# Optimization experiments

Hardware: AMD Instinct MI355X
Metric: run time of the kernel (lower is better)

## Reference

```python
import jax, jax.numpy as jnp
import numpy as np

R = 16       # voxel resolution
CH = 64      # channels
NSAMPLE = 16
PROJ = 3


def _bn(x, p, eps):
    # p: [4, C] rows = (gamma, beta, running_mean, running_var); eval-mode BN
    g, b, m, v = p
    sh = [1] * x.ndim
    sh[1] = -1
    return (x - m.reshape(sh)) * (g.reshape(sh) * jax.lax.rsqrt(v.reshape(sh) + eps)) + b.reshape(sh)


def _gather_ch(x, flat_idx):
    # x: [B, C, M], flat_idx: [B, L] -> [B, C, L]
    B, C, _ = x.shape
    idx = jnp.broadcast_to(flat_idx[:, None, :], (B, C, flat_idx.shape[1]))
    return jnp.take_along_axis(x, idx, axis=2)


def _pvb_forward(x, xyz, idx, w3d1, b3d1, bn3d1, w3d2, b3d2, bn3d2, proj_w1, proj_bn, proj_w2, pt_bn):
    B, C, N = x.shape
    r = R
    # ---------- voxelization (coords detached, normalize=False) ----------
    nc = xyz - xyz.mean(axis=2, keepdims=True)
    nc = jnp.clip((nc + 1.0) * 0.5 * r, 0.0, r - 1.0)
    nc = jax.lax.stop_gradient(nc)                        # [B,3,N] float in [0, r-1]
    vi = jnp.round(nc).astype(jnp.int32)
    flat = (vi[:, 0] * r + vi[:, 1]) * r + vi[:, 2]       # [B,N]
    seg = (flat + jnp.arange(B, dtype=jnp.int32)[:, None] * (r ** 3)).reshape(-1)
    feats = x.transpose(0, 2, 1).reshape(B * N, C)
    sums = jax.ops.segment_sum(feats, seg, num_segments=B * r ** 3)
    cnts = jax.ops.segment_sum(jnp.ones((B * N,), x.dtype), seg, num_segments=B * r ** 3)
    v = (sums / jnp.maximum(cnts, 1.0)[:, None]).reshape(B, r, r, r, C).transpose(0, 4, 1, 2, 3)
    # ---------- depthwise Conv3d -> BN3d -> LeakyReLU (x2) ----------
    dn = ('NCDHW', 'OIDHW', 'NCDHW')
    v = jax.lax.conv_general_dilated(v, w3d1, (1, 1, 1), 'SAME', dimension_numbers=dn,
                                     feature_group_count=C) + b3d1.reshape(1, C, 1, 1, 1)
    v = jax.nn.leaky_relu(_bn(v, bn3d1, 1e-4), 0.1)
    v = jax.lax.conv_general_dilated(v, w3d2, (1, 1, 1), 'SAME', dimension_numbers=dn,
                                     feature_group_count=C) + b3d2.reshape(1, C, 1, 1, 1)
    v = jax.nn.leaky_relu(_bn(v, bn3d2, 1e-4), 0.1)
    # ---------- trilinear devoxelize ----------
    vf = v.reshape(B, C, r ** 3)
    lo = jnp.floor(nc).astype(jnp.int32)
    fr = nc - lo
    hi = jnp.minimum(lo + 1, r - 1)
    p_v_x = jnp.zeros((B, C, N), x.dtype)
    for dx in (0, 1):
        for dy in (0, 1):
            for dz in (0, 1):
                xi = hi[:, 0] if dx else lo[:, 0]
                yi = hi[:, 1] if dy else lo[:, 1]
                zi = hi[:, 2] if dz else lo[:, 2]
                w = ((fr[:, 0] if dx else 1.0 - fr[:, 0]) *
                     (fr[:, 1] if dy else 1.0 - fr[:, 1]) *
                     (fr[:, 2] if dz else 1.0 - fr[:, 2]))
                p_v_x = p_v_x + w[:, None, :] * _gather_ch(vf, (xi * r + yi) * r + zi)
    # ---------- neighbor gather (precomputed ball-query idx) ----------
    K = idx.shape[-1]
    flat_nb = idx.reshape(B, N * K)
    x_j = _gather_ch(x, flat_nb).reshape(B, C, N, K)
    xyz_j = _gather_ch(xyz, flat_nb).reshape(B, 3, N, K)
    dp1 = xyz_j - xyz[:, :, :, None]                      # [B,3,N,K]
    df = x_j - x[:, :, :, None]                           # [B,C,N,K]
    # proj_conv: 1x1 conv -> BN2d -> ReLU -> 1x1 conv
    h = jnp.einsum('oc,bcnk->bonk', proj_w1, df)
    h = jax.nn.relu(_bn(h, proj_bn, 1e-5))
    dp2 = jnp.einsum('oc,bcnk->bonk', proj_w2, h)         # [B,3,N,K]
    dp = jnp.concatenate([dp1, dp2], axis=1)              # [B,6,N,K]
    # repeat_interleave of the 6 channels up to C (last gets remainder)
    part = 6
    rep = C // part
    repeats = np.array([rep] * (part - 1) + [C - rep * (part - 1)])
    w = jnp.repeat(dp, repeats, axis=1, total_repeat_length=C)
    x_j = x_j * w
    x_j = jax.nn.relu(_bn(x_j, pt_bn, 1e-5))              # proj_transform
    p_p_x = x_j.max(axis=-1)                              # max-pool over neighbors
    return p_v_x + p_p_x                                  # agg_way == 'add'


def setup_inputs() -> dict:
    key = jax.random.key(0)
    ks = jax.random.split(key, 16)
    B, C, N, K = 4, CH, 16384, NSAMPLE

    def bn_params(k, c):
        k1, k2, k3, k4 = jax.random.split(k, 4)
        return jnp.stack([1.0 + 0.1 * jax.random.normal(k1, (c,), jnp.float32),
                          0.1 * jax.random.normal(k2, (c,), jnp.float32),
                          0.1 * jax.random.normal(k3, (c,), jnp.float32),
                          jax.random.uniform(k4, (c,), jnp.float32, 0.5, 1.5)])

    return dict(
        x=jax.random.normal(ks[0], (B, C, N), jnp.float32),
        xyz=jax.random.uniform(ks[1], (B, 3, N), jnp.float32, -1.0, 1.0),
        idx=jax.random.randint(ks[2], (B, N, K), 0, N, jnp.int32),
        w3d1=0.1 * jax.random.normal(ks[3], (C, 1, 3, 3, 3), jnp.float32),
        b3d1=0.01 * jax.random.normal(ks[4], (C,), jnp.float32),
        bn3d1=bn_params(ks[5], C),
        w3d2=0.1 * jax.random.normal(ks[6], (C, 1, 3, 3, 3), jnp.float32),
        b3d2=0.01 * jax.random.normal(ks[7], (C,), jnp.float32),
        bn3d2=bn_params(ks[8], C),
        proj_w1=0.1 * jax.random.normal(ks[9], (PROJ, C), jnp.float32),
        proj_bn=bn_params(ks[10], PROJ),
        proj_w2=0.3 * jax.random.normal(ks[11], (PROJ, PROJ), jnp.float32),
        pt_bn=bn_params(ks[12], C),
    )


def reference(x, xyz, idx, w3d1, b3d1, bn3d1, w3d2, b3d2, bn3d2, proj_w1, proj_bn, proj_w2, pt_bn):
    return _pvb_forward(x, xyz, idx, w3d1, b3d1, bn3d1, w3d2, b3d2, bn3d2, proj_w1, proj_bn, proj_w2, pt_bn)
```

## Files before the change

### kernel.cpp

```cpp
#include <hip/hip_runtime.h>

namespace {
constexpr int B_  = 4;
constexpr int C_  = 64;
constexpr int N_  = 16384;
constexpr int K_  = 16;
constexpr int R3_ = 4096;

constexpr int OFF_MEANS = 0;
constexpr int OFF_XT    = 16;
constexpr int OFF_PTS   = OFF_XT  + B_*N_*C_/2;
constexpr int OFF_SUMS  = OFF_PTS + B_*N_*8;
constexpr int OFF_CNTS  = OFF_SUMS + B_*R3_*C_;
constexpr int OFF_VOX2  = OFF_CNTS + B_*R3_;
constexpr int FILL_FLOATS = B_*R3_*C_ + B_*R3_;
constexpr int FILL_BLOCKS = FILL_FLOATS / (256 * 4);
}

__device__ __forceinline__ unsigned short f2bf(float f) {
  unsigned u = __float_as_uint(f);
  return (unsigned short)((u + 0x7FFFu + ((u >> 16) & 1u)) >> 16);
}
__device__ __forceinline__ float bf2f(unsigned short h) {
  return __uint_as_float(((unsigned)h) << 16);
}
__device__ __forceinline__ unsigned cvtpk_bf16(float lo, float hi) {
  unsigned r;
  asm("v_cvt_pk_bf16_f32 %0, %1, %2" : "=v"(r) : "v"(lo), "v"(hi));
  return r;
}

__global__ __launch_bounds__(256) void k_init(
    const float* __restrict__ xyz, float* __restrict__ means,
    float* __restrict__ fill) {
  const int blk = blockIdx.x;
  if (blk >= 12) {
    const int base = (blk - 12) * (256 * 4) + threadIdx.x * 4;
    *(float4*)(fill + base) = make_float4(0.f, 0.f, 0.f, 0.f);
    return;
  }
  __shared__ double red[256];
  const float* p = xyz + blk * N_;
  double s = 0.0;
  for (int i = threadIdx.x; i < N_; i += 256) s += (double)p[i];
  red[threadIdx.x] = s;
  __syncthreads();
  for (int st = 128; st; st >>= 1) {
    if (threadIdx.x < st) red[threadIdx.x] += red[threadIdx.x + st];
    __syncthreads();
  }
  if (threadIdx.x == 0) means[blk] = (float)(red[0] * (1.0 / (double)N_));
}

__global__ __launch_bounds__(256) void k_prep(
    const float* __restrict__ x, const float* __restrict__ xyz,
    const float* __restrict__ pw1, const float* __restrict__ means,
    unsigned short* __restrict__ xT, float* __restrict__ pts,
    float* __restrict__ sums, float* __restrict__ cnts) {
  __shared__ float tile[64 * 65];
  __shared__ float ncs[3][64];
  __shared__ int   flats[64];

  const int t   = threadIdx.x;
  const int blk = blockIdx.x;
  const int b   = blk >> 8;
  const int n0  = (blk & 255) << 6;

#pragma unroll
  for (int i = 0; i < 16; ++i) {
    int c = i * 4 + (t >> 6);
    int j = t & 63;
    tile[c * 65 + j] = x[((size_t)(b * C_ + c)) * N_ + n0 + j];
  }
  __syncthreads();

#pragma unroll
  for (int i = 0; i < 16; ++i) {
    int p = i * 4 + (t >> 6);
    int c = t & 63;
    xT[((size_t)(b * N_ + n0 + p)) * C_ + c] = f2bf(tile[c * 65 + p]);
  }

  if (t < 192) {
    int p = t & 63, q = t >> 6;
    float s = 0.f;
#pragma unroll
    for (int c = 0; c < 64; ++c) s = fmaf(pw1[q * 64 + c], tile[c * 65 + p], s);
    size_t pb = ((size_t)(b * N_ + n0 + p)) * 8;
    pts[pb + 3 + q] = s;
    float v = xyz[((size_t)(b * 3 + q)) * N_ + n0 + p];
    pts[pb + q] = v;
    float nc = fminf(fmaxf((v - means[b * 3 + q] + 1.0f) * 8.0f, 0.0f), 15.0f);
    ncs[q][p] = nc;
  } else {
    int p = t & 63;
    size_t pb = ((size_t)(b * N_ + n0 + p)) * 8;
    pts[pb + 6] = 0.f;
    pts[pb + 7] = 0.f;
  }
  __syncthreads();

  if (t < 64) {
    int vx = (int)rintf(ncs[0][t]);
    int vy = (int)rintf(ncs[1][t]);
    int vz = (int)rintf(ncs[2][t]);
    int f = (vx * 16 + vy) * 16 + vz;
    flats[t] = f;
    atomicAdd(&cnts[b * R3_ + f], 1.0f);
  }
  __syncthreads();

  const int w = t >> 6, lane = t & 63;
#pragma unroll
  for (int i = 0; i < 16; ++i) {
    int p = w * 16 + i;
    int f = flats[p];
    atomicAdd(&sums[((size_t)(b * R3_ + f)) * C_ + lane], tile[lane * 65 + p]);
  }
}

__global__ __launch_bounds__(256) void k_conv(
    const float* __restrict__ sums, const float* __restrict__ cnts,
    const float* __restrict__ w3d1, const float* __restrict__ b3d1,
    const float* __restrict__ bn1, const float* __restrict__ w3d2,
    const float* __restrict__ b3d2, const float* __restrict__ bn2,
    unsigned short* __restrict__ vox2) {
  __shared__ float va[18 * 18 * 18];
  __shared__ float vb[18 * 18 * 18];
  const int t = threadIdx.x;
  const int b = blockIdx.x >> 6;
  const int c = blockIdx.x & 63;

  float W1[27], W2[27];
#pragma unroll
  for (int i = 0; i < 27; ++i) { W1[i] = w3d1[c * 27 + i]; W2[i] = w3d2[c * 27 + i]; }
  float s1 = bn1[c] / sqrtf(bn1[192 + c] + 1e-4f);
  float d1 = (b3d1[c] - bn1[128 + c]) * s1 + bn1[64 + c];
  float s2 = bn2[c] / sqrtf(bn2[192 + c] + 1e-4f);
  float d2 = (b3d2[c] - bn2[128 + c]) * s2 + bn2[64 + c];

  for (int i = t; i < 18 * 18 * 18; i += 256) { va[i] = 0.f; vb[i] = 0.f; }
  __syncthreads();

#pragma unroll
  for (int i = 0; i < 16; ++i) {
    int vox = t + i * 256;
    int z = vox & 15, y = (vox >> 4) & 15, xx = vox >> 8;
    float cnt = cnts[b * R3_ + vox];
    float v = sums[((size_t)(b * R3_ + vox)) * C_ + c] / fmaxf(cnt, 1.0f);
    va[((xx + 1) * 18 + (y + 1)) * 18 + (z + 1)] = v;
  }
  __syncthreads();

#pragma unroll
  for (int i = 0; i < 16; ++i) {
    int vox = t + i * 256;
    int z = vox & 15, y = (vox >> 4) & 15, xx = vox >> 8;
    int base = ((xx + 1) * 18 + (y + 1)) * 18 + (z + 1);
    float acc = 0.f;
#pragma unroll
    for (int dx = -1; dx <= 1; ++dx)
#pragma unroll
      for (int dy = -1; dy <= 1; ++dy)
#pragma unroll
        for (int dz = -1; dz <= 1; ++dz)
          acc = fmaf(W1[((dx + 1) * 3 + (dy + 1)) * 3 + (dz + 1)],
                     va[base + dx * 324 + dy * 18 + dz], acc);
    float tt = acc * s1 + d1;
    vb[base] = tt > 0.f ? tt : 0.1f * tt;
  }
  __syncthreads();

#pragma unroll
  for (int i = 0; i < 16; ++i) {
    int vox = t + i * 256;
    int z = vox & 15, y = (vox >> 4) & 15, xx = vox >> 8;
    int base = ((xx + 1) * 18 + (y + 1)) * 18 + (z + 1);
    float acc = 0.f;
#pragma unroll
    for (int dx = -1; dx <= 1; ++dx)
#pragma unroll
      for (int dy = -1; dy <= 1; ++dy)
#pragma unroll
        for (int dz = -1; dz <= 1; ++dz)
          acc = fmaf(W2[((dx + 1) * 3 + (dy + 1)) * 3 + (dz + 1)],
                     vb[base + dx * 324 + dy * 18 + dz], acc);
    float tt = acc * s2 + d2;
    vox2[((size_t)(b * R3_ + vox)) * C_ + c] = f2bf(tt > 0.f ? tt : 0.1f * tt);
  }
}

__global__ __launch_bounds__(256, 8) void k_final(
    const unsigned short* __restrict__ xT, const float* __restrict__ pts,
    const unsigned short* __restrict__ vox2, const int* __restrict__ idx,
    const float* __restrict__ means, const float* __restrict__ pbn,
    const float* __restrict__ pw2, const float* __restrict__ ptbn,
    float* __restrict__ out) {
  __shared__ unsigned w6[3][513];
  __shared__ int      jarr[512];
  __shared__ unsigned dv[32][8];
  __shared__ float    outT[64 * 33];

  const int t = threadIdx.x;
  const int blk = blockIdx.x;
  const int xcd = blk & 7;
  const int b = xcd >> 1;
  const int t32 = ((blk >> 3) << 1) | (xcd & 1);
  const int n0 = t32 * 32;

  const float psc0 = pbn[0] * rsqrtf(pbn[9]  + 1e-5f);
  const float psc1 = pbn[1] * rsqrtf(pbn[10] + 1e-5f);
  const float psc2 = pbn[2] * rsqrtf(pbn[11] + 1e-5f);
  const float pof0 = pbn[3] - pbn[6] * psc0;
  const float pof1 = pbn[4] - pbn[7] * psc1;
  const float pof2 = pbn[5] - pbn[8] * psc2;
  float W2r[9];
#pragma unroll
  for (int i = 0; i < 9; ++i) W2r[i] = pw2[i];

  const float* __restrict__ ptsb = pts + (size_t)b * N_ * 8;

#pragma unroll
  for (int rep = 0; rep < 2; ++rep) {
    const int q = t + rep * 256;
    const int p = q >> 4;
    const int n = n0 + p;
    const int j = idx[(size_t)b * N_ * K_ + (size_t)n0 * K_ + q];
    jarr[q] = j;
    const float* qr = ptsb + (size_t)j * 8;
    float4 qa = *(const float4*)qr;
    float4 qb = *(const float4*)(qr + 4);
    const float* ir = ptsb + (size_t)n * 8;
    float4 pa = *(const float4*)ir;
    float4 pb = *(const float4*)(ir + 4);
    float d0 = qa.x - pa.x, d1 = qa.y - pa.y, d2 = qa.z - pa.z;
    float c0 = pof0 - psc0 * pa.w;
    float c1 = pof1 - psc1 * pb.x;
    float c2 = pof2 - psc2 * pb.y;
    float h0 = fmaxf(fmaf(qa.w, psc0, c0), 0.f);
    float h1 = fmaxf(fmaf(qb.x, psc1, c1), 0.f);
    float h2 = fmaxf(fmaf(qb.y, psc2, c2), 0.f);
    float e0 = fmaf(W2r[0], h0, fmaf(W2r[1], h1, W2r[2] * h2));
    float e1 = fmaf(W2r[3], h0, fmaf(W2r[4], h1, W2r[5] * h2));
    float e2 = fmaf(W2r[6], h0, fmaf(W2r[7], h1, W2r[8] * h2));
    w6[0][q] = cvtpk_bf16(d0, d1);
    w6[1][q] = cvtpk_bf16(d2, e0);
    w6[2][q] = cvtpk_bf16(e1, e2);
  }

  if (t < 32) {
    const int n = n0 + t;
    const float* ir = ptsb + (size_t)n * 8;
    float x0 = ir[0], x1 = ir[1], x2 = ir[2];
    float nc0 = fminf(fmaxf((x0 - means[b * 3 + 0] + 1.0f) * 8.0f, 0.0f), 15.0f);
    float nc1 = fminf(fmaxf((x1 - means[b * 3 + 1] + 1.0f) * 8.0f, 0.0f), 15.0f);
    float nc2 = fminf(fmaxf((x2 - means[b * 3 + 2] + 1.0f) * 8.0f, 0.0f), 15.0f);
    int lx = (int)nc0, ly = (int)nc1, lz = (int)nc2;
    float fx = nc0 - (float)lx, fy = nc1 - (float)ly, fz = nc2 - (float)lz;
    int hx = lx < 15 ? lx + 1 : 15;
    int hy = ly < 15 ? ly + 1 : 15;
    int hz = lz < 15 ? lz + 1 : 15;
    float wx[2] = {1.f - fx, fx};
    float wy[2] = {1.f - fy, fy};
    float wz[2] = {1.f - fz, fz};
    int xi[2] = {lx, hx}, yi[2] = {ly, hy}, zi[2] = {lz, hz};
#pragma unroll
    for (int c8 = 0; c8 < 8; ++c8) {
      int dx = c8 >> 2, dy = (c8 >> 1) & 1, dz = c8 & 1;
      int flat = (xi[dx] * 16 + yi[dy]) * 16 + zi[dz];
      float wt = wx[dx] * wy[dy] * wz[dz];
      dv[t][c8] = ((unsigned)flat << 16) | (unsigned)f2bf(wt);
    }
  }
  __syncthreads();

  const int w = t >> 6, lane = t & 63;
  const int widx = lane < 20 ? 0 : lane < 40 ? 1 : 2;
  const bool hi = (lane >= 10 && lane < 20) || (lane >= 30 && lane < 40) || (lane >= 50);
  const float ts = ptbn[lane] * rsqrtf(ptbn[192 + lane] + 1e-5f);
  const float td = ptbn[64 + lane] - ptbn[128 + lane] * ts;
  const unsigned short* __restrict__ xTb = xT + (size_t)b * N_ * C_;
  const unsigned short* __restrict__ voxb = vox2 + (size_t)b * R3_ * C_;

#pragma unroll
  for (int i = 0; i < 8; ++i) {
    const int p = i * 4 + w;

    float acc = 0.f;
#pragma unroll
    for (int c8 = 0; c8 < 8; ++c8) {
      unsigned dvv = dv[p][c8];
      float wt = __uint_as_float(dvv << 16);
      acc = fmaf(wt, bf2f(voxb[(size_t)(dvv >> 16) * C_ + lane]), acc);
    }

    float pm = 0.f;
    const unsigned* w6p = &w6[widx][p * 16];
#pragma unroll
    for (int k = 0; k < 16; ++k) {
      const int j = jarr[p * 16 + k];
      const unsigned short xj = xTb[(size_t)j * C_ + lane];
      const unsigned wvp = w6p[k];
      float wf = hi ? __uint_as_float(wvp & 0xffff0000u)
                    : __uint_as_float(wvp << 16);
      float v = bf2f(xj) * wf;
      pm = fmaxf(pm, fmaf(v, ts, td));
    }

    outT[lane * 33 + p] = acc + pm;
  }
  __syncthreads();

#pragma unroll
  for (int i = 0; i < 8; ++i) {
    int c = i * 8 + (t >> 5);
    int col = t & 31;
    out[((size_t)(b * C_ + c)) * N_ + n0 + col] = outT[c * 33 + col];
  }
}

extern "C" void kernel_launch(void* const* d_in, const int* in_sizes, int n_in,
                              void* d_out, int out_size, void* d_ws, size_t ws_size,
                              hipStream_t stream) {
  const float* x     = (const float*)d_in[0];
  const float* xyz   = (const float*)d_in[1];
  const int*   idx   = (const int*)  d_in[2];
  const float* w3d1  = (const float*)d_in[3];
  const float* b3d1  = (const float*)d_in[4];
  const float* bn3d1 = (const float*)d_in[5];
  const float* w3d2  = (const float*)d_in[6];
  const float* b3d2  = (const float*)d_in[7];
  const float* bn3d2 = (const float*)d_in[8];
  const float* pw1   = (const float*)d_in[9];
  const float* pbn   = (const float*)d_in[10];
  const float* pw2   = (const float*)d_in[11];
  const float* ptbn  = (const float*)d_in[12];
  float* out = (float*)d_out;
  float* ws  = (float*)d_ws;

  k_init<<<dim3(12 + FILL_BLOCKS), dim3(256), 0, stream>>>(
      xyz, ws + OFF_MEANS, ws + OFF_SUMS);
  k_prep<<<dim3(B_ * N_ / 64), dim3(256), 0, stream>>>(
      x, xyz, pw1, ws + OFF_MEANS, (unsigned short*)(ws + OFF_XT), ws + OFF_PTS,
      ws + OFF_SUMS, ws + OFF_CNTS);
  k_conv<<<dim3(B_ * C_), dim3(256), 0, stream>>>(
      ws + OFF_SUMS, ws + OFF_CNTS, w3d1, b3d1, bn3d1, w3d2, b3d2, bn3d2,
      (unsigned short*)(ws + OFF_VOX2));
  k_final<<<dim3(B_ * N_ / 32), dim3(256), 0, stream>>>(
      (const unsigned short*)(ws + OFF_XT), ws + OFF_PTS,
      (const unsigned short*)(ws + OFF_VOX2), idx, ws + OFF_MEANS,
      pbn, pw2, ptbn, out);
}
```

Before: 92.73 us.

## Add transpose kernel for voxel grid and batch gathers in final kernel

Adds a k_tr kernel that transposes the voxel sums from voxel-major to channel-major layout and folds the count normalization into it. k_conv then reads each channel row contiguously instead of with a 64-float stride. In k_final, all 8 trilinear and 16 neighbor gathers are issued up front so the loads overlap, and the hi/lo bf16 select becomes a single shift. The cost is one extra kernel launch and an extra 4 MB round trip through memory.

Result: faster. 90.07 us (-2.9%).

```diff
diff --git a/kernel.cpp b/kernel.cpp
--- a/kernel.cpp
+++ b/kernel.cpp
@@ -12,7 +12,8 @@
 constexpr int OFF_PTS   = OFF_XT  + B_*N_*C_/2;
 constexpr int OFF_SUMS  = OFF_PTS + B_*N_*8;
 constexpr int OFF_CNTS  = OFF_SUMS + B_*R3_*C_;
-constexpr int OFF_VOX2  = OFF_CNTS + B_*R3_;
+constexpr int OFF_VT    = OFF_CNTS + B_*R3_;
+constexpr int OFF_VOX2  = OFF_VT   + B_*C_*R3_;
 constexpr int FILL_FLOATS = B_*R3_*C_ + B_*R3_;
 constexpr int FILL_BLOCKS = FILL_FLOATS / (256 * 4);
 }
@@ -119,8 +120,32 @@
   }
 }
 
+__global__ __launch_bounds__(256) void k_tr(
+    const float* __restrict__ sums, const float* __restrict__ cnts,
+    float* __restrict__ vT) {
+  __shared__ float tile[64 * 65];
+  const int t = threadIdx.x;
+  const int b = blockIdx.x >> 6;
+  const int v0 = (blockIdx.x & 63) << 6;
+
+#pragma unroll
+  for (int i = 0; i < 16; ++i) {
+    int r = i * 4 + (t >> 6);
+    int c = t & 63;
+    tile[r * 65 + c] = sums[((size_t)(b * R3_ + v0 + r)) * C_ + c];
+  }
+  const float rcnt = 1.0f / fmaxf(cnts[b * R3_ + v0 + (t & 63)], 1.0f);
+  __syncthreads();
+#pragma unroll
+  for (int i = 0; i < 16; ++i) {
+    int c = i * 4 + (t >> 6);
+    int r = t & 63;
+    vT[((size_t)(b * C_ + c)) * R3_ + v0 + r] = tile[r * 65 + c] * rcnt;
+  }
+}
+
 __global__ __launch_bounds__(256) void k_conv(
-    const float* __restrict__ sums, const float* __restrict__ cnts,
+    const float* __restrict__ vT,
     const float* __restrict__ w3d1, const float* __restrict__ b3d1,
     const float* __restrict__ bn1, const float* __restrict__ w3d2,
     const float* __restrict__ b3d2, const float* __restrict__ bn2,
@@ -134,21 +159,20 @@
   float W1[27], W2[27];
 #pragma unroll
   for (int i = 0; i < 27; ++i) { W1[i] = w3d1[c * 27 + i]; W2[i] = w3d2[c * 27 + i]; }
-  float s1 = bn1[c] / sqrtf(bn1[192 + c] + 1e-4f);
-  float d1 = (b3d1[c] - bn1[128 + c]) * s1 + bn1[64 + c];
-  float s2 = bn2[c] / sqrtf(bn2[192 + c] + 1e-4f);
-  float d2 = (b3d2[c] - bn2[128 + c]) * s2 + bn2[64 + c];
+  const float s1 = bn1[c] / sqrtf(bn1[192 + c] + 1e-4f);
+  const float d1 = (b3d1[c] - bn1[128 + c]) * s1 + bn1[64 + c];
+  const float s2 = bn2[c] / sqrtf(bn2[192 + c] + 1e-4f);
+  const float d2 = (b3d2[c] - bn2[128 + c]) * s2 + bn2[64 + c];
 
   for (int i = t; i < 18 * 18 * 18; i += 256) { va[i] = 0.f; vb[i] = 0.f; }
+  const float* __restrict__ vrow = vT + ((size_t)(b * C_ + c)) * R3_;
   __syncthreads();
 
 #pragma unroll
   for (int i = 0; i < 16; ++i) {
     int vox = t + i * 256;
     int z = vox & 15, y = (vox >> 4) & 15, xx = vox >> 8;
-    float cnt = cnts[b * R3_ + vox];
-    float v = sums[((size_t)(b * R3_ + vox)) * C_ + c] / fmaxf(cnt, 1.0f);
-    va[((xx + 1) * 18 + (y + 1)) * 18 + (z + 1)] = v;
+    va[((xx + 1) * 18 + (y + 1)) * 18 + (z + 1)] = vrow[vox];
   }
   __syncthreads();
 
@@ -277,6 +301,7 @@
   const int w = t >> 6, lane = t & 63;
   const int widx = lane < 20 ? 0 : lane < 40 ? 1 : 2;
   const bool hi = (lane >= 10 && lane < 20) || (lane >= 30 && lane < 40) || (lane >= 50);
+  const unsigned shl = hi ? 0u : 16u;
   const float ts = ptbn[lane] * rsqrtf(ptbn[192 + lane] + 1e-5f);
   const float td = ptbn[64 + lane] - ptbn[128 + lane] * ts;
   const unsigned short* __restrict__ xTb = xT + (size_t)b * N_ * C_;
@@ -285,26 +310,27 @@
 #pragma unroll
   for (int i = 0; i < 8; ++i) {
     const int p = i * 4 + w;
+    const int pq = p * 16;
+
+    unsigned short vxv[8];
+#pragma unroll
+    for (int c8 = 0; c8 < 8; ++c8)
+      vxv[c8] = voxb[(size_t)(dv[p][c8] >> 16) * C_ + lane];
+    unsigned short xjv[16];
+#pragma unroll
+    for (int k = 0; k < 16; ++k)
+      xjv[k] = xTb[(size_t)jarr[pq + k] * C_ + lane];
 
     float acc = 0.f;
 #pragma unroll
-    for (int c8 = 0; c8 < 8; ++c8) {
-      unsigned dvv = dv[p][c8];
-      float wt = __uint_as_float(dvv << 16);
-      acc = fmaf(wt, bf2f(voxb[(size_t)(dvv >> 16) * C_ + lane]), acc);
-    }
+    for (int c8 = 0; c8 < 8; ++c8)
+      acc = fmaf(__uint_as_float(dv[p][c8] << 16), bf2f(vxv[c8]), acc);
 
     float pm = 0.f;
-    const unsigned* w6p = &w6[widx][p * 16];
 #pragma unroll
     for (int k = 0; k < 16; ++k) {
-      const int j = jarr[p * 16 + k];
-      const unsigned short xj = xTb[(size_t)j * C_ + lane];
-      const unsigned wvp = w6p[k];
-      float wf = hi ? __uint_as_float(wvp & 0xffff0000u)
-                    : __uint_as_float(wvp << 16);
-      float v = bf2f(xj) * wf;
-      pm = fmaxf(pm, fmaf(v, ts, td));
+      float wf = __uint_as_float(w6[widx][pq + k] << shl);
+      pm = fmaxf(pm, fmaf(bf2f(xjv[k]) * wf, ts, td));
     }
 
     outT[lane * 33 + p] = acc + pm;
@@ -343,8 +369,10 @@
   k_prep<<<dim3(B_ * N_ / 64), dim3(256), 0, stream>>>(
       x, xyz, pw1, ws + OFF_MEANS, (unsigned short*)(ws + OFF_XT), ws + OFF_PTS,
       ws + OFF_SUMS, ws + OFF_CNTS);
+  k_tr<<<dim3(B_ * 64), dim3(256), 0, stream>>>(
+      ws + OFF_SUMS, ws + OFF_CNTS, ws + OFF_VT);
   k_conv<<<dim3(B_ * C_), dim3(256), 0, stream>>>(
-      ws + OFF_SUMS, ws + OFF_CNTS, w3d1, b3d1, bn3d1, w3d2, b3d2, bn3d2,
+      ws + OFF_VT, w3d1, b3d1, bn3d1, w3d2, b3d2, bn3d2,
       (unsigned short*)(ws + OFF_VOX2));
   k_final<<<dim3(B_ * N_ / 32), dim3(256), 0, stream>>>(
       (const unsigned short*)(ws + OFF_XT), ws + OFF_PTS,
```
